# Performance work log

Measured on AMD Instinct MI355X. Metric: run time of the kernel, lower is better.

## Reference

```python
import jax, jax.numpy as jnp
import numpy as np

C = 64; K = 3; KS = 7; A = 16
B, H, W = 4, 128, 128
EXTEND_SCOPE = 1.0
EPS = 1e-5

def _dct_mats(n):
    k = np.arange(n)[:, None]; m = np.arange(n)[None, :]
    D = 2.0 * np.cos(np.pi * (2 * m + 1) * k / (2.0 * n))  # torch_dct DCT-II, norm=None
    return jnp.asarray(D, jnp.float32), jnp.asarray(np.linalg.inv(D), jnp.float32)

_D, _Dinv = _dct_mats(K)

def _conv2d(x, w, b=None, stride=(1, 1), padding='SAME', groups=1):
    y = jax.lax.conv_general_dilated(x, w, stride, padding, feature_group_count=groups, dimension_numbers=('NCHW', 'OIHW', 'NCHW'))
    return y if b is None else y + b[None, :, None, None]

def _dwt(x):
    x1 = x[:, :, 0::2, 0::2] * 0.5; x2 = x[:, :, 1::2, 0::2] * 0.5
    x3 = x[:, :, 0::2, 1::2] * 0.5; x4 = x[:, :, 1::2, 1::2] * 0.5
    return (x1 + x2 + x3 + x4, -x1 + x2 - x3 + x4, -x1 - x2 + x3 + x4, x1 - x2 - x3 + x4)

def _iwt(LL, LH, HL, HH):
    a, b_, c, d = LL * 0.5, LH * 0.5, HL * 0.5, HH * 0.5
    n, ch, h, w = LL.shape
    out = jnp.zeros((n, ch, 2 * h, 2 * w), LL.dtype)
    out = out.at[:, :, 0::2, 0::2].set(a - b_ - c + d)
    out = out.at[:, :, 1::2, 0::2].set(a + b_ - c - d)
    out = out.at[:, :, 0::2, 1::2].set(a - b_ + c - d)
    out = out.at[:, :, 1::2, 1::2].set(a + b_ + c + d)
    return out

def _omni(x, fc_w, bn_g, bn_b, bn_m, bn_v, ch_w, ch_b, fl_w, fl_b, sp_w=None, sp_b=None):
    g = x.mean((2, 3))                                   # global avg pool -> [B,C]
    a = g @ fc_w.T
    a = jax.nn.relu((a - bn_m) * jax.lax.rsqrt(bn_v + EPS) * bn_g + bn_b)  # BN (eval)
    c_att = jax.nn.sigmoid(a @ ch_w.T + ch_b)
    f_att = jax.nn.sigmoid(a @ fl_w.T + fl_b)
    sp_att = None if sp_w is None else jax.nn.sigmoid(a @ sp_w.T + sp_b)
    return c_att, f_att, sp_att

def _forward(x, weight, ratio, o1_fc_w, o1_bn_g, o1_bn_b, o1_bn_m, o1_bn_v, o1_ch_w, o1_ch_b, o1_fl_w, o1_fl_b, o2_fc_w, o2_bn_g, o2_bn_b, o2_bn_m, o2_bn_v, o2_ch_w, o2_ch_b, o2_fl_w, o2_fl_b, o2_sp_w, o2_sp_b, off_w, off_b, obn_g, obn_b, obn_m, obn_v, ds_w, ds_b, gn_g, gn_b):
    b = x.shape[0]
    LL, LH, HL, HH = _dwt(x)
    c1, f1, _ = _omni(x, o1_fc_w, o1_bn_g, o1_bn_b, o1_bn_m, o1_bn_v, o1_ch_w, o1_ch_b, o1_fl_w, o1_fl_b)
    c2, f2, sp2 = _omni(x, o2_fc_w, o2_bn_g, o2_bn_b, o2_bn_m, o2_bn_v, o2_ch_w, o2_ch_b, o2_fl_w, o2_fl_b, o2_sp_w, o2_sp_b)
    # adaptive frequency-modulated dynamic kernels
    aw = jnp.broadcast_to(weight[None], (b,) + weight.shape)        # [B,Co,Ci,K,K]
    awm = aw.mean((-1, -2), keepdims=True)
    awr = aw - awm
    dctc = jnp.einsum('km,bojmn,ln->bojkl', _D, awr, _D)            # dct_2d
    dctc = dctc * (sp2.reshape(b, 1, 1, K, K) * 2.0)
    awr = jnp.einsum('km,bojmn,ln->bojkl', _Dinv, dctc, _Dinv)      # idct_2d
    aw = ratio * (awm * (c1[:, None, :, None, None] * 2) * (f1[:, :, None, None, None] * 2)) + (1.0 - ratio) * (awr * (c2[:, None, :, None, None] * 2) * (f2[:, :, None, None, None] * 2))
    # grouped conv (groups=b*C) then sum over c_in == depthwise conv with kernels summed over c_in (Cin==Cout)
    weff = aw.sum(axis=2)                                           # [B,C,K,K]
    h2, w2 = HH.shape[2], HH.shape[3]
    hh = _conv2d(HH.reshape(1, b * C, h2, w2), weff.reshape(b * C, 1, K, K), groups=b * C).reshape(b, C, h2, w2)
    out = _iwt(LL, LH, HL, hh) + x
    # ---- DSConv (dynamic snake conv, morph=0) ----
    off = _conv2d(out, off_w, off_b)
    off = (off - obn_m[None, :, None, None]) * jax.lax.rsqrt(obn_v + EPS)[None, :, None, None] * obn_g[None, :, None, None] + obn_b[None, :, None, None]
    y_off = jnp.tanh(off)[:, :KS]                                   # [B,KS,H,W]
    center = KS // 2
    low = jnp.flip(jnp.cumsum(jnp.flip(y_off[:, :center], 1), 1), 1)
    up = jnp.cumsum(y_off[:, center + 1:], 1)
    dy = jnp.concatenate([low, jnp.zeros_like(y_off[:, :1]), up], 1) * EXTEND_SCOPE
    hh_, ww_ = out.shape[2], out.shape[3]
    rows = jnp.clip(jnp.arange(hh_, dtype=x.dtype)[None, None, :, None] + dy, 0.0, hh_ - 1.0)
    cols = jnp.arange(ww_, dtype=x.dtype)[None, None, None, :] + (jnp.arange(KS, dtype=x.dtype) - center)[None, :, None, None]
    cols = jnp.clip(jnp.broadcast_to(cols, rows.shape), 0.0, ww_ - 1.0)
    r0 = jnp.floor(rows); c0 = jnp.floor(cols)
    wr = (rows - r0)[:, None]; wc = (cols - c0)[:, None]            # [B,1,KS,H,W]
    r0i = r0.astype(jnp.int32); c0i = c0.astype(jnp.int32)
    r1i = jnp.minimum(r0i + 1, hh_ - 1); c1i = jnp.minimum(c0i + 1, ww_ - 1)
    samp = jax.vmap(lambda img, ri, ci: img[:, ri, ci])             # [C,H,W],[KS,H,W] -> [C,KS,H,W]
    g00 = samp(out, r0i, c0i); g01 = samp(out, r0i, c1i)
    g10 = samp(out, r1i, c0i); g11 = samp(out, r1i, c1i)
    deform = (1 - wr) * (1 - wc) * g00 + (1 - wr) * wc * g01 + wr * (1 - wc) * g10 + wr * wc * g11
    deform = deform.transpose(0, 1, 3, 2, 4).reshape(b, C, hh_ * KS, ww_)
    y = _conv2d(deform, ds_w, ds_b, stride=(KS, 1), padding='VALID')  # [B,C,H,W]
    G = C // 4                                                       # GroupNorm(out//4)
    z = y.reshape(b, G, C // G, hh_, ww_)
    mu = z.mean((2, 3, 4), keepdims=True)
    var = ((z - mu) ** 2).mean((2, 3, 4), keepdims=True)
    y = ((z - mu) * jax.lax.rsqrt(var + EPS)).reshape(b, C, hh_, ww_)
    return jax.nn.relu(y * gn_g[None, :, None, None] + gn_b[None, :, None, None])

def setup_inputs() -> dict:
    key = jax.random.key(0)
    ks = jax.random.split(key, 12)
    def n(k, shape, s): return jax.random.normal(k, shape, jnp.float32) * s
    return dict(
        x=jax.random.normal(ks[0], (B, C, H, W), jnp.float32),
        weight=n(ks[1], (C, C, K, K), 0.1),
        ratio=jnp.asarray(0.5, jnp.float32),
        o1_fc_w=n(ks[2], (A, C), 0.2), o1_bn_g=jnp.ones((A,), jnp.float32), o1_bn_b=jnp.zeros((A,), jnp.float32),
        o1_bn_m=jnp.zeros((A,), jnp.float32), o1_bn_v=jnp.ones((A,), jnp.float32),
        o1_ch_w=n(ks[3], (C, A), 0.2), o1_ch_b=jnp.zeros((C,), jnp.float32),
        o1_fl_w=n(ks[4], (C, A), 0.2), o1_fl_b=jnp.zeros((C,), jnp.float32),
        o2_fc_w=n(ks[5], (A, C), 0.2), o2_bn_g=jnp.ones((A,), jnp.float32), o2_bn_b=jnp.zeros((A,), jnp.float32),
        o2_bn_m=jnp.zeros((A,), jnp.float32), o2_bn_v=jnp.ones((A,), jnp.float32),
        o2_ch_w=n(ks[6], (C, A), 0.2), o2_ch_b=jnp.zeros((C,), jnp.float32),
        o2_fl_w=n(ks[7], (C, A), 0.2), o2_fl_b=jnp.zeros((C,), jnp.float32),
        o2_sp_w=n(ks[8], (K * K, A), 0.2), o2_sp_b=jnp.zeros((K * K,), jnp.float32),
        off_w=n(ks[9], (2 * KS, C, 3, 3), 0.05), off_b=jnp.zeros((2 * KS,), jnp.float32),
        obn_g=jnp.ones((2 * KS,), jnp.float32), obn_b=jnp.zeros((2 * KS,), jnp.float32),
        obn_m=jnp.zeros((2 * KS,), jnp.float32), obn_v=jnp.ones((2 * KS,), jnp.float32),
        ds_w=n(ks[10], (C, C, KS, 1), 0.05), ds_b=jnp.zeros((C,), jnp.float32),
        gn_g=jnp.ones((C,), jnp.float32), gn_b=jnp.zeros((C,), jnp.float32),
    )

def reference(x, weight, ratio, o1_fc_w, o1_bn_g, o1_bn_b, o1_bn_m, o1_bn_v, o1_ch_w, o1_ch_b, o1_fl_w, o1_fl_b, o2_fc_w, o2_bn_g, o2_bn_b, o2_bn_m, o2_bn_v, o2_ch_w, o2_ch_b, o2_fl_w, o2_fl_b, o2_sp_w, o2_sp_b, off_w, off_b, obn_g, obn_b, obn_m, obn_v, ds_w, ds_b, gn_g, gn_b):
    return _forward(x, weight, ratio, o1_fc_w, o1_bn_g, o1_bn_b, o1_bn_m, o1_bn_v, o1_ch_w, o1_ch_b, o1_fl_w, o1_fl_b, o2_fc_w, o2_bn_g, o2_bn_b, o2_bn_m, o2_bn_v, o2_ch_w, o2_ch_b, o2_fl_w, o2_fl_b, o2_sp_w, o2_sp_b, off_w, off_b, obn_g, obn_b, obn_m, obn_v, ds_w, ds_b, gn_g, gn_b)
```

## Files before the change

### kernel.cpp

```cpp
#include <hip/hip_runtime.h>
#include <math.h>

#define BB 4
#define CC 64
#define HH_ 128
#define WW 128
#define HPW (HH_*WW)
#define KH 64
#define KW 64
#define KSZ 7
#define AA 16
#define EPSV 1e-5f
#define KTOT 448

typedef __attribute__((ext_vector_type(8))) short bf16x8;
typedef __attribute__((ext_vector_type(4))) float f32x4;
typedef unsigned short ushort_t;

__device__ __forceinline__ float sigm(float x){ return 1.0f/(1.0f+expf(-x)); }
__device__ __forceinline__ unsigned short f2bf(float f){
  unsigned u = __float_as_uint(f);
  return (unsigned short)((u + 0x7fffu + ((u>>16)&1u)) >> 16);
}

__global__ __launch_bounds__(512) void k_dwt0(const float* __restrict__ x,
  const float* __restrict__ dsw, const float* __restrict__ offw,
  float* __restrict__ HHb, float* __restrict__ partial,
  ushort_t* __restrict__ dsWbf, ushort_t* __restrict__ offAbf)
{
  int t = threadIdx.x; int wg = blockIdx.x;
  int idx = wg*512 + t;
  if(idx < CC*KTOT){
    int co = idx/KTOT; int K = idx%KTOT; int k = K>>6; int ci = K&63;
    dsWbf[idx] = f2bf(dsw[(size_t)(co*CC+ci)*KSZ + k]);
  } else {
    int j2 = idx - CC*KTOT;
    if(j2 < 18*16*32){
      int kl = j2&31; int co = (j2>>5)&15; int s = j2>>9;
      int tap = s>>1; int ci = (s&1)*32 + kl;
      float v = 0.f;
      if(co<KSZ) v = offw[((size_t)co*CC + ci)*9 + tap];
      offAbf[j2] = f2bf(v);
    }
  }
  int lane = t&63, wid = t>>6;
  int e0 = wg*2048 + t*4;
  int bc = e0>>12; int h2 = (e0>>6)&63; int w0 = e0&63;
  const float* xp = x + (size_t)bc*HPW;
  float4 a0 = *(const float4*)(xp + (2*h2)*WW + 2*w0);
  float4 a1 = *(const float4*)(xp + (2*h2)*WW + 2*w0 + 4);
  float4 b0 = *(const float4*)(xp + (2*h2+1)*WW + 2*w0);
  float4 b1 = *(const float4*)(xp + (2*h2+1)*WW + 2*w0 + 4);
  float4 hh;
  hh.x = 0.5f*(a0.x - b0.x - a0.y + b0.y);
  hh.y = 0.5f*(a0.z - b0.z - a0.w + b0.w);
  hh.z = 0.5f*(a1.x - b1.x - a1.y + b1.y);
  hh.w = 0.5f*(a1.z - b1.z - a1.w + b1.w);
  *(float4*)(HHb + e0) = hh;
  float s = a0.x+a0.y+a0.z+a0.w + a1.x+a1.y+a1.z+a1.w
          + b0.x+b0.y+b0.z+b0.w + b1.x+b1.y+b1.z+b1.w;
  for(int o=32;o>0;o>>=1) s += __shfl_down(s,o);
  __shared__ float ls[8];
  if(lane==0) ls[wid] = s;
  __syncthreads();
  if(t==0){
    float tot=0.f;
    #pragma unroll
    for(int k2=0;k2<8;k2++) tot += ls[k2];
    partial[wg] = tot;
  }
}

__global__ __launch_bounds__(64) void k_weff2(const float* __restrict__ partial,
  const float* __restrict__ w, const float* __restrict__ ratio_p,
  const float* __restrict__ o1fc, const float* __restrict__ o1g,const float* __restrict__ o1b,
  const float* __restrict__ o1m,const float* __restrict__ o1v,
  const float* __restrict__ o1cw,const float* __restrict__ o1cb,
  const float* __restrict__ o1fw,const float* __restrict__ o1fb,
  const float* __restrict__ o2fc, const float* __restrict__ o2g,const float* __restrict__ o2b,
  const float* __restrict__ o2m,const float* __restrict__ o2v,
  const float* __restrict__ o2cw,const float* __restrict__ o2cb,
  const float* __restrict__ o2fw,const float* __restrict__ o2fb,
  const float* __restrict__ spw,const float* __restrict__ spb,
  float* __restrict__ weff)
{
  int bo = blockIdx.x; int b = bo>>6, o = bo&63; int ci = threadIdx.x;
  int bc = b*CC+ci;
  float g_own = (partial[2*bc] + partial[2*bc+1]) * (1.0f/HPW);
  float d1=o1cb[ci], d2=o1fb[ci], d3=o2cb[ci], d4=o2fb[ci];
  float sspacc[9];
  #pragma unroll
  for(int e=0;e<9;e++) sspacc[e]=spb[e];
  for(int j=0;j<AA;j++){
    float p1 = g_own * o1fc[j*CC+ci];
    float p2 = g_own * o2fc[j*CC+ci];
    #pragma unroll
    for(int off=32;off>0;off>>=1){ p1+=__shfl_xor(p1,off); p2+=__shfl_xor(p2,off); }
    p1 = (p1-o1m[j])*rsqrtf(o1v[j]+EPSV)*o1g[j]+o1b[j]; p1=fmaxf(p1,0.f);
    p2 = (p2-o2m[j])*rsqrtf(o2v[j]+EPSV)*o2g[j]+o2b[j]; p2=fmaxf(p2,0.f);
    d1 += p1*o1cw[ci*AA+j]; d2 += p1*o1fw[ci*AA+j];
    d3 += p2*o2cw[ci*AA+j]; d4 += p2*o2fw[ci*AA+j];
    #pragma unroll
    for(int e=0;e<9;e++) sspacc[e] += p2*spw[e*AA+j];
  }
  float sc1v=sigm(d1), sc2v=sigm(d3);
  float sf1o=__shfl(sigm(d2),o), sf2o=__shfl(sigm(d4),o);
  const float* wp = w + (size_t)(o*CC+ci)*9;
  float w9[9]; float m=0.f;
  #pragma unroll
  for(int e=0;e<9;e++){ w9[e]=wp[e]; m+=w9[e]; }
  m *= (1.0f/9.0f);
  float S1 = m * sc1v;
  float M[9];
  #pragma unroll
  for(int e=0;e<9;e++) M[e] = (w9[e]-m)*sc2v;
  #pragma unroll
  for(int off=32; off>0; off>>=1){
    S1 += __shfl_xor(S1, off);
    #pragma unroll
    for(int e=0;e<9;e++) M[e] += __shfl_xor(M[e], off);
  }
  if(ci==0){
    const float Dm[3][3] = {{2.f,2.f,2.f},{1.7320508075688772f,0.f,-1.7320508075688772f},{1.f,-2.f,1.f}};
    const float Di[3][3] = {{0.16666666666666666f,0.28867513459481287f,0.16666666666666666f},
                            {0.16666666666666666f,0.f,-0.3333333333333333f},
                            {0.16666666666666666f,-0.28867513459481287f,0.16666666666666666f}};
    float U[3][3], T[3][3], V[3][3], R[3][3];
    for(int k=0;k<3;k++)for(int n=0;n<3;n++) U[k][n]=Dm[k][0]*M[0*3+n]+Dm[k][1]*M[1*3+n]+Dm[k][2]*M[2*3+n];
    for(int k=0;k<3;k++)for(int l=0;l<3;l++) T[k][l]=(U[k][0]*Dm[l][0]+U[k][1]*Dm[l][1]+U[k][2]*Dm[l][2])*2.0f*sigm(sspacc[k*3+l]);
    for(int k=0;k<3;k++)for(int n=0;n<3;n++) V[k][n]=Di[k][0]*T[0][n]+Di[k][1]*T[1][n]+Di[k][2]*T[2][n];
    for(int k=0;k<3;k++)for(int l=0;l<3;l++) R[k][l]=V[k][0]*Di[l][0]+V[k][1]*Di[l][1]+V[k][2]*Di[l][2];
    float rr = ratio_p[0];
    float base = rr*4.0f*sf1o*S1;
    float w2f = (1.0f-rr)*4.0f*sf2o;
    #pragma unroll
    for(int e=0;e<9;e++) weff[(size_t)bo*9+e] = base + w2f*R[e/3][e%3];
  }
}

__global__ __launch_bounds__(256) void k_iwtT(const float* __restrict__ HHb,
  const float* __restrict__ x, const float* __restrict__ weff,
  float* __restrict__ outT, ushort_t* __restrict__ outTbf)
{
  __shared__ __align__(16) char smem[33024 + 16640];
  float* hs  = (float*)smem;
  float* xt  = (float*)smem;
  float* d_s = (float*)(smem + 33024);
  int wg = blockIdx.x; int b = wg>>7, h = wg&127; int h2 = h>>1;
  int t = threadIdx.x;
  #pragma unroll
  for(int half=0; half<2; ++half){
    for(int e=t; e<32*3*66; e+=256){
      int c_l = e/198; int rem = e - c_l*198; int r3 = rem/66; int wz = rem - r3*66;
      int r = h2 - 1 + r3; int w2 = wz - 1;
      int c = half*32 + c_l;
      float v = 0.f;
      if(r>=0 && r<KH && w2>=0 && w2<KW)
        v = HHb[((size_t)(b*CC+c))*(KH*KW) + r*KW + w2];
      hs[(c_l*3 + r3)*66 + wz] = v;
    }
    __syncthreads();
    {
      int c_l = t>>3, q = t&7;
      int c = half*32 + c_l;
      float wk[9];
      #pragma unroll
      for(int e=0;e<9;e++) wk[e] = weff[(size_t)(b*CC+c)*9+e];
      const float* hb = hs + c_l*198;
      #pragma unroll
      for(int j=0;j<8;j++){
        int w2 = q*8+j;
        float conv = 0.f;
        #pragma unroll
        for(int dh=0;dh<3;dh++){
          const float* hr = hb + dh*66 + w2;
          conv += wk[dh*3+0]*hr[0] + wk[dh*3+1]*hr[1] + wk[dh*3+2]*hr[2];
        }
        d_s[c*65+w2] = 0.5f*(conv - hb[1*66 + w2 + 1]);
      }
    }
    __syncthreads();
  }
  for(int e=t; e<CC*WW; e+=256){
    int cc=e>>7, w=e&127;
    xt[cc*129+w] = x[((size_t)(b*CC+cc)*HH_+h)*WW + w];
  }
  __syncthreads();
  float* dst = outT + ((size_t)(b*HH_+h))*WW*CC;
  ushort_t* dstb = outTbf + ((size_t)(b*HH_+h))*130*CC;
  for(int e=t; e<CC*WW; e+=256){
    int w=e>>6, cc=e&63;
    float dv = d_s[cc*65+(w>>1)];
    float val = 2.f*xt[cc*129+w] + (((h + w)&1) ? -dv : dv);
    dst[e] = val;
    dstb[(w+1)*CC + cc] = f2bf(val);
  }
  if(t<128){ int cc=t&63; int side=t>>6; dstb[(size_t)side*129*CC + cc] = 0; }
}

__global__ __launch_bounds__(512) void k_dsfused(const float* __restrict__ outT,
  const ushort_t* __restrict__ outTbf, const ushort_t* __restrict__ dsWbf,
  const ushort_t* __restrict__ offAbf, const float* __restrict__ offb,
  const float* __restrict__ obg, const float* __restrict__ obb,
  const float* __restrict__ obm, const float* __restrict__ obv,
  const float* __restrict__ dsb, float* __restrict__ yout, float* __restrict__ pstats)
{
  __shared__ ushort_t S2a[2*8192];
  __shared__ int sb0[KSZ*128], sb1[KSZ*128];
  __shared__ float swr[KSZ*128];
  __shared__ float off_s[KSZ*128];
  __shared__ float dy_s[KSZ*128];
  int t = threadIdx.x;
  int wg = blockIdx.x; int sw = (wg&7)*64 + (wg>>3);
  int b = sw>>7, h = sw&127;
  int lane = t&63, wid = t>>6;
  int arow = lane&15, kgrp = lane>>4;
  {
    f32x4 acc = (f32x4){0.f,0.f,0.f,0.f};
    #pragma unroll
    for(int s=0;s<18;s++){
      int tap = s>>1, chalf = s&1;
      int r = tap/3, dwp = tap%3;
      int hr = h - 1 + r;
      if(hr<0 || hr>=HH_) continue;
      bf16x8 aF = *(const bf16x8*)(offAbf + (s*16+arow)*32 + kgrp*8);
      const ushort_t* base = outTbf + ((size_t)(b*HH_+hr))*130*CC + chalf*32 + kgrp*8;
      int wp = (wid<<4) + arow + dwp;
      bf16x8 bF = *(const bf16x8*)(base + (size_t)wp*CC);
      acc = __builtin_amdgcn_mfma_f32_16x16x32_bf16(aF, bF, acc, 0,0,0);
    }
    #pragma unroll
    for(int r=0;r<4;r++){
      int co = kgrp*4+r;
      if(co<KSZ) off_s[co*128 + (wid<<4) + arow] = acc[r];
    }
  }
  __syncthreads();
  if(t<128){
    int w = t;
    float y[KSZ];
    #pragma unroll
    for(int k=0;k<KSZ;k++){
      float sc = obg[k]*rsqrtf(obv[k]+EPSV);
      float sh = obb[k]-obm[k]*sc;
      y[k] = tanhf((off_s[k*128+w]+offb[k])*sc+sh);
    }
    dy_s[      w]=y[0]+y[1]+y[2]; dy_s[128+w]=y[1]+y[2]; dy_s[256+w]=y[2];
    dy_s[384+w]=0.f; dy_s[512+w]=y[4]; dy_s[640+w]=y[4]+y[5]; dy_s[768+w]=y[4]+y[5]+y[6];
  }
  __syncthreads();
  for(int e=t; e<KSZ*128; e+=512){
    int k = e>>7, w = e&127;
    float dv = dy_s[e];
    float r = fminf(fmaxf((float)h + dv, 0.f), 127.f);
    float rf = floorf(r); int r0=(int)rf; float wr=r-rf; int r1=min(r0+1,127);
    int c = min(max(w+k-3,0),127);
    sb0[k*128+w] = ((b*HH_+r0)*WW+c)*CC;
    sb1[k*128+w] = ((b*HH_+r1)*WW+c)*CC;
    swr[k*128+w] = wr;
  }
  __syncthreads();
  int cg2 = wid&3, wh = wid>>2;
  {
    ushort_t* buf = S2a;
    #pragma unroll
    for(int i=0;i<16;i++){
      int p = (wid<<4)+i;
      int b0=sb0[p], b1=sb1[p]; float wr=swr[p];
      float av = outT[b0+lane], c2 = outT[b1+lane];
      float v = av + wr*(c2-av);
      int idx = (p<<6)|lane;
      buf[idx ^ ((p&7)<<3)] = f2bf(v);
    }
  }
  __syncthreads();
  f32x4 acc[4];
  #pragma unroll
  for(int nt=0;nt<4;nt++) acc[nt] = (f32x4){0.f,0.f,0.f,0.f};
  int bufs = 0;
  for(int k=0;k<KSZ;k++){
    const ushort_t* Wp = dsWbf + (size_t)((cg2<<4)+arow)*KTOT + (k<<6) + kgrp*8;
    bf16x8 a0 = *(const bf16x8*)Wp;
    bf16x8 a1 = *(const bf16x8*)(Wp+32);
    if(k+1<KSZ){
      ushort_t* nb = S2a + (bufs^1)*8192;
      #pragma unroll
      for(int i=0;i<16;i++){
        int p = (wid<<4)+i;
        int b0=sb0[(k+1)*128+p], b1=sb1[(k+1)*128+p]; float wr=swr[(k+1)*128+p];
        float av = outT[b0+lane], c2 = outT[b1+lane];
        float v = av + wr*(c2-av);
        int idx = (p<<6)|lane;
        nb[idx ^ ((p&7)<<3)] = f2bf(v);
      }
    }
    const ushort_t* cb = S2a + bufs*8192;
    #pragma unroll
    for(int nt=0;nt<4;nt++){
      int pos = (wh<<6) + (nt<<4) + arow;
      int i0 = (pos<<6) + kgrp*8;
      int sz = (pos&7)<<3;
      bf16x8 b0 = *(const bf16x8*)(cb + (i0 ^ sz));
      bf16x8 b1 = *(const bf16x8*)(cb + ((i0+32) ^ sz));
      acc[nt] = __builtin_amdgcn_mfma_f32_16x16x32_bf16(a0, b0, acc[nt], 0,0,0);
      acc[nt] = __builtin_amdgcn_mfma_f32_16x16x32_bf16(a1, b1, acc[nt], 0,0,0);
    }
    __syncthreads();
    bufs ^= 1;
  }
  float vs[4]={0.f,0.f,0.f,0.f}, vq[4]={0.f,0.f,0.f,0.f};
  #pragma unroll
  for(int r=0;r<4;r++){
    int co = (cg2<<4) + kgrp*4 + r;
    float bias = dsb[co];
    #pragma unroll
    for(int nt=0;nt<4;nt++){
      float y = acc[nt][r] + bias;
      int wcol = (wh<<6) + (nt<<4) + arow;
      yout[((size_t)(b*CC+co)*HH_ + h)*WW + wcol] = y;
      vs[r] += y; vq[r] += y*y;
    }
  }
  #pragma unroll
  for(int m=1;m<16;m<<=1){
    #pragma unroll
    for(int r=0;r<4;r++){ vs[r]+=__shfl_xor(vs[r],m); vq[r]+=__shfl_xor(vq[r],m); }
  }
  if(arow==0){
    #pragma unroll
    for(int r=0;r<4;r++){
      int co = (cg2<<4)+kgrp*4+r;
      int pi = (b*CC+co)*256 + h*2 + wh;
      pstats[pi] = vs[r];
      pstats[65536+pi] = vq[r];
    }
  }
}

__global__ __launch_bounds__(256) void k_gnfin2(const float* __restrict__ pstats,
                                                float* __restrict__ gstat){
  int bg = blockIdx.x; int b = bg>>4, g = bg&15; int t = threadIdx.x;
  float s=0.f, q=0.f;
  #pragma unroll
  for(int c4=0;c4<4;c4++){
    int base = (b*CC + g*4+c4)*256;
    s += pstats[base + t];
    q += pstats[65536 + base + t];
  }
  for(int o=32;o>0;o>>=1){ s+=__shfl_down(s,o); q+=__shfl_down(q,o); }
  __shared__ float ls[4], lq[4];
  if((t&63)==0){ ls[t>>6]=s; lq[t>>6]=q; }
  __syncthreads();
  if(t==0){
    float S=ls[0]+ls[1]+ls[2]+ls[3], Q=lq[0]+lq[1]+lq[2]+lq[3];
    float inv = 1.0f/(4.0f*HPW);
    float mu = S*inv; float var = Q*inv - mu*mu;
    gstat[bg*2]=mu; gstat[bg*2+1]=rsqrtf(var+EPSV);
  }
}

__global__ void k_gnapply(float* __restrict__ y, const float* __restrict__ gstat,
  const float* __restrict__ gg, const float* __restrict__ gb){
  int idx = blockIdx.x*256 + threadIdx.x;
  float4* p = (float4*)y;
  int bc = idx >> 12;
  int b = bc>>6, c = bc&63;
  int gi = b*16 + (c>>2);
  float mu = gstat[gi*2], rstd = gstat[gi*2+1];
  float sc = rstd*gg[c], sh = gb[c]-mu*sc;
  float4 v = p[idx];
  v.x = fmaxf(v.x*sc+sh, 0.f);
  v.y = fmaxf(v.y*sc+sh, 0.f);
  v.z = fmaxf(v.z*sc+sh, 0.f);
  v.w = fmaxf(v.w*sc+sh, 0.f);
  p[idx] = v;
}

extern "C" void kernel_launch(void* const* d_in, const int* in_sizes, int n_in,
                              void* d_out, int out_size, void* d_ws, size_t ws_size,
                              hipStream_t stream) {
  const float* x      = (const float*)d_in[0];
  const float* weight = (const float*)d_in[1];
  const float* ratio  = (const float*)d_in[2];
  const float* o1fc   = (const float*)d_in[3];
  const float* o1g    = (const float*)d_in[4];
  const float* o1b    = (const float*)d_in[5];
  const float* o1m    = (const float*)d_in[6];
  const float* o1v    = (const float*)d_in[7];
  const float* o1cw   = (const float*)d_in[8];
  const float* o1cb   = (const float*)d_in[9];
  const float* o1fw   = (const float*)d_in[10];
  const float* o1fb   = (const float*)d_in[11];
  const float* o2fc   = (const float*)d_in[12];
  const float* o2g    = (const float*)d_in[13];
  const float* o2b    = (const float*)d_in[14];
  const float* o2m    = (const float*)d_in[15];
  const float* o2v    = (const float*)d_in[16];
  const float* o2cw   = (const float*)d_in[17];
  const float* o2cb   = (const float*)d_in[18];
  const float* o2fw   = (const float*)d_in[19];
  const float* o2fb   = (const float*)d_in[20];
  const float* spw    = (const float*)d_in[21];
  const float* spb    = (const float*)d_in[22];
  const float* offw   = (const float*)d_in[23];
  const float* offb   = (const float*)d_in[24];
  const float* obg    = (const float*)d_in[25];
  const float* obb    = (const float*)d_in[26];
  const float* obm    = (const float*)d_in[27];
  const float* obv    = (const float*)d_in[28];
  const float* dsw    = (const float*)d_in[29];
  const float* dsb    = (const float*)d_in[30];
  const float* gng    = (const float*)d_in[31];
  const float* gnb    = (const float*)d_in[32];

  float* ws    = (float*)d_ws;
  float* HHb   = ws;
  float* partial = ws + 1048576;
  float* weff  = ws + 1049088;
  float* gstat = ws + 1051392;
  ushort_t* dsWbf  = (ushort_t*)(ws + 1051520);
  ushort_t* offAbf = (ushort_t*)(ws + 1065856);
  float* pstats= ws + 1070464;
  float* outT  = ws + 1201536;
  ushort_t* outTbf = (ushort_t*)(ws + 5395840);
  float* outb  = (float*)d_out;

  k_dwt0<<<512,512,0,stream>>>(x, dsw, offw, HHb, partial, dsWbf, offAbf);
  k_weff2<<<256,64,0,stream>>>(partial, weight, ratio,
    o1fc,o1g,o1b,o1m,o1v,o1cw,o1cb,o1fw,o1fb,
    o2fc,o2g,o2b,o2m,o2v,o2cw,o2cb,o2fw,o2fb,
    spw,spb, weff);
  k_iwtT<<<512,256,0,stream>>>(HHb, x, weff, outT, outTbf);
  k_dsfused<<<512,512,0,stream>>>(outT, outTbf, dsWbf, offAbf,
    offb, obg, obb, obm, obv, dsb, outb, pstats);
  k_gnfin2<<<64,256,0,stream>>>(pstats, gstat);
  k_gnapply<<<4096,256,0,stream>>>(outb, gstat, gng, gnb);
}
```

Measured before the change: 95.87 us.

## Share iwt conv across row pairs and vectorize deformable gather loads

The iwtT kernel now handles two output rows (h=2*h2 and 2*h2+1) per block. Both rows use the same half-resolution conv result d_s, so the HH halo loads and the 3x3 conv run half as often, at the cost of half as many blocks. In k_dsfused the bilinear gather now has each lane load float4 from both source rows and write packed bf16x4 into the swizzled LDS tile, replacing scalar per-lane loads. The weight fragment loads move inside the nt loop, which may add redundant global or cache traffic and change register pressure.

```diff
diff --git a/kernel.cpp b/kernel.cpp
--- a/kernel.cpp
+++ b/kernel.cpp
@@ -146,7 +146,7 @@
   float* hs  = (float*)smem;
   float* xt  = (float*)smem;
   float* d_s = (float*)(smem + 33024);
-  int wg = blockIdx.x; int b = wg>>7, h = wg&127; int h2 = h>>1;
+  int wg = blockIdx.x; int b = wg>>6, h2 = wg&63;
   int t = threadIdx.x;
   #pragma unroll
   for(int half=0; half<2; ++half){
@@ -181,21 +181,26 @@
     }
     __syncthreads();
   }
-  for(int e=t; e<CC*WW; e+=256){
-    int cc=e>>7, w=e&127;
-    xt[cc*129+w] = x[((size_t)(b*CC+cc)*HH_+h)*WW + w];
-  }
-  __syncthreads();
-  float* dst = outT + ((size_t)(b*HH_+h))*WW*CC;
-  ushort_t* dstb = outTbf + ((size_t)(b*HH_+h))*130*CC;
-  for(int e=t; e<CC*WW; e+=256){
-    int w=e>>6, cc=e&63;
-    float dv = d_s[cc*65+(w>>1)];
-    float val = 2.f*xt[cc*129+w] + (((h + w)&1) ? -dv : dv);
-    dst[e] = val;
-    dstb[(w+1)*CC + cc] = f2bf(val);
-  }
-  if(t<128){ int cc=t&63; int side=t>>6; dstb[(size_t)side*129*CC + cc] = 0; }
+  #pragma unroll
+  for(int r=0;r<2;r++){
+    int h = 2*h2 + r;
+    for(int e=t; e<CC*WW; e+=256){
+      int cc=e>>7, w=e&127;
+      xt[cc*129+w] = x[((size_t)(b*CC+cc)*HH_+h)*WW + w];
+    }
+    __syncthreads();
+    float* dst = outT + ((size_t)(b*HH_+h))*WW*CC;
+    ushort_t* dstb = outTbf + ((size_t)(b*HH_+h))*130*CC;
+    for(int e=t; e<CC*WW; e+=256){
+      int w=e>>6, cc=e&63;
+      float dv = d_s[cc*65+(w>>1)];
+      float val = 2.f*xt[cc*129+w] + (((h + w)&1) ? -dv : dv);
+      dst[e] = val;
+      dstb[(w+1)*CC + cc] = f2bf(val);
+    }
+    if(t<128){ int cc=t&63; int side=t>>6; dstb[(size_t)side*129*CC + cc] = 0; }
+    __syncthreads();
+  }
 }
 
 __global__ __launch_bounds__(512) void k_dsfused(const float* __restrict__ outT,
@@ -261,16 +266,20 @@
   }
   __syncthreads();
   int cg2 = wid&3, wh = wid>>2;
+  int rsub = lane>>4;
+  int ciq  = (lane&15)<<2;
   {
     ushort_t* buf = S2a;
     #pragma unroll
-    for(int i=0;i<16;i++){
-      int p = (wid<<4)+i;
-      int b0=sb0[p], b1=sb1[p]; float wr=swr[p];
-      float av = outT[b0+lane], c2 = outT[b1+lane];
-      float v = av + wr*(c2-av);
-      int idx = (p<<6)|lane;
-      buf[idx ^ ((p&7)<<3)] = f2bf(v);
+    for(int i=0;i<4;i++){
+      int p = (wid<<4) + i*4 + rsub;
+      float4 v0 = *(const float4*)(outT + sb0[p] + ciq);
+      float4 v1 = *(const float4*)(outT + sb1[p] + ciq);
+      float wr = swr[p];
+      unsigned lo = (unsigned)f2bf(v0.x + wr*(v1.x-v0.x)) | ((unsigned)f2bf(v0.y + wr*(v1.y-v0.y))<<16);
+      unsigned hi = (unsigned)f2bf(v0.z + wr*(v1.z-v0.z)) | ((unsigned)f2bf(v0.w + wr*(v1.w-v0.w))<<16);
+      int off = (p*128 + ciq*2) ^ ((p&7)<<4);
+      *(uint2*)((char*)buf + off) = make_uint2(lo,hi);
     }
   }
   __syncthreads();
@@ -279,19 +288,19 @@
   for(int nt=0;nt<4;nt++) acc[nt] = (f32x4){0.f,0.f,0.f,0.f};
   int bufs = 0;
   for(int k=0;k<KSZ;k++){
-    const ushort_t* Wp = dsWbf + (size_t)((cg2<<4)+arow)*KTOT + (k<<6) + kgrp*8;
-    bf16x8 a0 = *(const bf16x8*)Wp;
-    bf16x8 a1 = *(const bf16x8*)(Wp+32);
     if(k+1<KSZ){
       ushort_t* nb = S2a + (bufs^1)*8192;
       #pragma unroll
-      for(int i=0;i<16;i++){
-        int p = (wid<<4)+i;
-        int b0=sb0[(k+1)*128+p], b1=sb1[(k+1)*128+p]; float wr=swr[(k+1)*128+p];
-        float av = outT[b0+lane], c2 = outT[b1+lane];
-        float v = av + wr*(c2-av);
-        int idx = (p<<6)|lane;
-        nb[idx ^ ((p&7)<<3)] = f2bf(v);
+      for(int i=0;i<4;i++){
+        int p = (wid<<4) + i*4 + rsub;
+        int e = (k+1)*128 + p;
+        float4 v0 = *(const float4*)(outT + sb0[e] + ciq);
+        float4 v1 = *(const float4*)(outT + sb1[e] + ciq);
+        float wr = swr[e];
+        unsigned lo = (unsigned)f2bf(v0.x + wr*(v1.x-v0.x)) | ((unsigned)f2bf(v0.y + wr*(v1.y-v0.y))<<16);
+        unsigned hi = (unsigned)f2bf(v0.z + wr*(v1.z-v0.z)) | ((unsigned)f2bf(v0.w + wr*(v1.w-v0.w))<<16);
+        int off = (p*128 + ciq*2) ^ ((p&7)<<4);
+        *(uint2*)((char*)nb + off) = make_uint2(lo,hi);
       }
     }
     const ushort_t* cb = S2a + bufs*8192;
@@ -302,6 +311,9 @@
       int sz = (pos&7)<<3;
       bf16x8 b0 = *(const bf16x8*)(cb + (i0 ^ sz));
       bf16x8 b1 = *(const bf16x8*)(cb + ((i0+32) ^ sz));
+      const ushort_t* Wp = dsWbf + (size_t)((cg2<<4)+arow)*KTOT + (k<<6) + kgrp*8;
+      bf16x8 a0 = *(const bf16x8*)Wp;
+      bf16x8 a1 = *(const bf16x8*)(Wp+32);
       acc[nt] = __builtin_amdgcn_mfma_f32_16x16x32_bf16(a0, b0, acc[nt], 0,0,0);
       acc[nt] = __builtin_amdgcn_mfma_f32_16x16x32_bf16(a1, b1, acc[nt], 0,0,0);
     }
@@ -430,7 +442,7 @@
     o1fc,o1g,o1b,o1m,o1v,o1cw,o1cb,o1fw,o1fb,
     o2fc,o2g,o2b,o2m,o2v,o2cw,o2cb,o2fw,o2fb,
     spw,spb, weff);
-  k_iwtT<<<512,256,0,stream>>>(HHb, x, weff, outT, outTbf);
+  k_iwtT<<<256,256,0,stream>>>(HHb, x, weff, outT, outTbf);
   k_dsfused<<<512,512,0,stream>>>(outT, outTbf, dsWbf, offAbf,
     offb, obg, obb, obm, obv, dsb, outb, pstats);
   k_gnfin2<<<64,256,0,stream>>>(pstats, gstat);
```

Result: no change. 94.75 us (-1.2%).
